# Kernel tuning notes

Measured on AMD Instinct MI355X. Metric: run time of the kernel, lower is better.

## Reference

```python
import jax, jax.numpy as jnp
import numpy as np

ALPHA = 0.65
KERNEL_RADIUS = 3
BIG = 1e30  # stand-in for +inf in morphological (tropical) convolution


def morphological_kernel(finsler_params, kernel_radius, alpha):
    """Sample the fractional morphological kernel on a (2r+1)x(2r+1) grid.

    F_c(x,y) = sqrt(x^2+y^2) * exp(-sum_k params[c,k] * B_k(theta)) with
    B_1=cos(t), B_2=sin(t), B_3=cos(2t), ... (circular harmonics).
    Kernel for the alpha-homogeneous HJB PDE (t=1):
      k(x) = nu_a * F(x)^(2a/(2a-1)),  nu_a = (2a-1)*(2a)^(-2a/(2a-1)).
    """
    r = kernel_radius
    coords = jnp.arange(-r, r + 1, dtype=finsler_params.dtype)
    yy = coords[:, None]  # [kh,1]
    xx = coords[None, :]  # [1,kw]
    rho = jnp.sqrt(xx * xx + yy * yy)              # [kh,kw]
    theta = jnp.arctan2(yy + 0 * xx, xx + 0 * yy)  # [kh,kw]
    K = finsler_params.shape[1]
    ks = np.arange(1, K + 1)
    freqs = jnp.asarray((ks + 1) // 2, dtype=finsler_params.dtype)  # 1,1,2,2,...
    ang = freqs[:, None, None] * theta[None]                        # [K,kh,kw]
    is_cos = jnp.asarray(ks % 2 == 1)[:, None, None]
    basis = jnp.where(is_cos, jnp.cos(ang), jnp.sin(ang))           # [K,kh,kw]
    F = rho[None] * jnp.exp(-jnp.einsum('ck,kij->cij', finsler_params, basis))  # [C,kh,kw]
    p = 2.0 * alpha / (2.0 * alpha - 1.0)
    nu = (2.0 * alpha - 1.0) * (2.0 * alpha) ** (-p)
    return nu * F ** p  # zero at origin since p>0


def morphological_convolution(u, kernel):
    """out[b,c,y,x] = min_{dy,dx} u[b,c,y+dy,x+dx] + kernel[c,dy+r,dx+r].
    Scan over the (2r+1)^2 stencil offsets with a running min (no huge patches)."""
    B, C, H, W = u.shape
    kh, kw = kernel.shape[1], kernel.shape[2]
    r = kh // 2
    pad = jnp.pad(u, ((0, 0), (0, 0), (r, r), (r, r)), constant_values=BIG)
    kflat = kernel.reshape(C, kh * kw)
    dys, dxs = jnp.meshgrid(jnp.arange(kh), jnp.arange(kw), indexing='ij')
    offs = jnp.stack([dys.reshape(-1), dxs.reshape(-1)], axis=-1)  # [kh*kw,2]

    def step(carry, i):
        dy, dx = offs[i, 0], offs[i, 1]
        sl = jax.lax.dynamic_slice(pad, (0, 0, dy, dx), (B, C, H, W))
        cand = sl + kflat[:, i][None, :, None, None]
        return jnp.minimum(carry, cand), None

    init = jnp.full((B, C, H, W), BIG, u.dtype)
    out, _ = jax.lax.scan(step, init, jnp.arange(kh * kw))
    return out


def convection(u, c):
    """Translation-equivariant transport: out(x) = u(x - c_channel), bilinear
    interpolation, replicate boundary. c[:,0]=x-shift, c[:,1]=y-shift."""
    B, C, H, W = u.shape
    gy = jnp.arange(H, dtype=u.dtype)[None, :, None] - c[:, 1][:, None, None]  # [C,H,1]
    gx = jnp.arange(W, dtype=u.dtype)[None, None, :] - c[:, 0][:, None, None]  # [C,1,W]
    y0 = jnp.floor(gy)
    x0 = jnp.floor(gx)
    wy = gy - y0  # [C,H,1]
    wx = gx - x0  # [C,1,W]
    y0i = jnp.clip(y0.astype(jnp.int32), 0, H - 1)
    y1i = jnp.clip(y0i + 1, 0, H - 1)
    x0i = jnp.clip(x0.astype(jnp.int32), 0, W - 1)
    x1i = jnp.clip(x0i + 1, 0, W - 1)
    ci = jnp.arange(C)[:, None, None]

    def gather(yi, xi):  # yi:[C,H,1], xi:[C,1,W] -> [B,C,H,W]
        return u[:, ci, yi, xi]

    return ((1 - wy) * (1 - wx) * gather(y0i, x0i)
            + (1 - wy) * wx * gather(y0i, x1i)
            + wy * (1 - wx) * gather(y1i, x0i)
            + wy * wx * gather(y1i, x1i))


def cde_pde_layer(x, c, finsler_dil, finsler_ero, weight):
    u = convection(x, c)
    k_dil = morphological_kernel(finsler_dil, KERNEL_RADIUS, ALPHA)
    u = -morphological_convolution(-u, k_dil)           # fractional dilation
    k_ero = morphological_kernel(finsler_ero, KERNEL_RADIUS, ALPHA)
    u = morphological_convolution(u, k_ero)             # fractional erosion
    return jnp.einsum('bihw,io->bohw', u, weight)       # linear channel mix


def setup_inputs() -> dict:
    key = jax.random.key(0)
    k1, k2, k3, k4, k5 = jax.random.split(key, 5)
    B, Cin, Cout, H, W, K = 16, 32, 32, 256, 256, 4
    x = jax.random.normal(k1, (B, Cin, H, W), dtype=jnp.float32)
    c = jax.random.normal(k2, (Cin, 2), dtype=jnp.float32)  # ~kaiming-uniform scale
    finsler_dil = jax.random.uniform(k3, (Cin, K), minval=-1.0, maxval=1.0, dtype=jnp.float32)
    finsler_ero = jax.random.uniform(k4, (Cin, K), minval=-1.0, maxval=1.0, dtype=jnp.float32)
    weight = jax.random.normal(k5, (Cin, Cout), dtype=jnp.float32) / np.sqrt(Cin)
    return {"x": x, "c": c, "finsler_dil": finsler_dil, "finsler_ero": finsler_ero, "weight": weight}


def reference(x, c, finsler_dil, finsler_ero, weight):
    return cde_pde_layer(x, c, finsler_dil, finsler_ero, weight)
```

## Files before the change

kernel.cpp:

```cpp
#include <hip/hip_runtime.h>
#include <math.h>

#define HH 256
#define WW 256
#define NB 16
#define NC 32
#define RAD 3
#define KWID 7
#define NTAPS 49
#define TILE 64
#define CW 76
#define CH 76
#define BUFH (CH * CW + 16)
#define BIGF 1e30f
#define PADF  -57344.0f
#define TAPCLAMP 57344.0f
#define HBB 0x7B80u

typedef _Float16 h2 __attribute__((ext_vector_type(2)));

static __device__ __forceinline__ h2 h2_u(unsigned int u) {
    union { unsigned int u; h2 h; } cv; cv.u = u; return cv.h;
}
static __device__ __forceinline__ unsigned int u_h2(h2 h) {
    union { unsigned int u; h2 h; } cv; cv.h = h; return cv.u;
}

__global__ void kgen_kernel(const float* __restrict__ fd,
                            const float* __restrict__ fe,
                            unsigned int* __restrict__ kd,
                            unsigned int* __restrict__ ke) {
    const int c = blockIdx.x;
    const int t = threadIdx.x;
    if (t >= NTAPS) return;
    const int dy = t / KWID - RAD;
    const int dx = t % KWID - RAD;
    const double rho = sqrt((double)(dx * dx + dy * dy));
    const double th  = atan2((double)dy, (double)dx);
    const double alpha = 0.65;
    const double p  = 2.0 * alpha / (2.0 * alpha - 1.0);
    const double nu = (2.0 * alpha - 1.0) * pow(2.0 * alpha, -p);
    const double b1 = cos(th), b2 = sin(th), b3 = cos(2.0 * th), b4 = sin(2.0 * th);
    double s, F;
    s = (double)fd[c * 4 + 0] * b1 + (double)fd[c * 4 + 1] * b2
      + (double)fd[c * 4 + 2] * b3 + (double)fd[c * 4 + 3] * b4;
    F = rho * exp(-s);
    {
        const float kv = fminf((float)(nu * pow(F, p)), TAPCLAMP);
        union { _Float16 h; unsigned short u; } cv; cv.h = (_Float16)(-kv);
        kd[c * NTAPS + t] = (unsigned int)cv.u | ((unsigned int)cv.u << 16);
    }
    s = (double)fe[c * 4 + 0] * b1 + (double)fe[c * 4 + 1] * b2
      + (double)fe[c * 4 + 2] * b3 + (double)fe[c * 4 + 3] * b4;
    F = rho * exp(-s);
    {
        const float kv = fminf((float)(nu * pow(F, p)), TAPCLAMP);
        union { _Float16 h; unsigned short u; } cv; cv.h = (_Float16)(kv);
        ke[c * NTAPS + t] = (unsigned int)cv.u | ((unsigned int)cv.u << 16);
    }
}

__global__ __launch_bounds__(256, 8) void cde_stencil_kernel(
    const float* __restrict__ xin, const float* __restrict__ csh,
    const unsigned int* __restrict__ kdil, const unsigned int* __restrict__ kero,
    float* __restrict__ uout)
{
    __shared__ __align__(16) _Float16 bufh[BUFH];

    const int tid = threadIdx.x;
    const int tileId = blockIdx.x;
    const int c = blockIdx.y;
    const int b = blockIdx.z;
    const int ty0 = (tileId >> 2) * TILE;
    const int tx0 = (tileId & 3) * TILE;

    const float cx = csh[c * 2 + 0];
    const float cy = csh[c * 2 + 1];
    const float* __restrict__ xb = xin + (((size_t)b * NC + c) << 16);

    const float mcx = -cx, mcy = -cy;
    const float fx0 = floorf(mcx), fy0 = floorf(mcy);
    const float wxf = mcx - fx0, wyf = mcy - fy0;
    const int IX = (int)fx0, IY = (int)fy0;
    const float w00 = (1.f - wyf) * (1.f - wxf);
    const float w01 = (1.f - wyf) * wxf;
    const float w10 = wyf * (1.f - wxf);
    const float w11 = wyf * wxf;

    {
        int row = tid / CW;
        int col = tid - row * CW;
        for (int idx = tid; idx < CH * CW; idx += 256) {
            const int gy = ty0 - 6 + row;
            const int gx = tx0 - 6 + col;
            float v = PADF;
            if (gy >= 0 && gy < HH && gx >= 0 && gx < WW) {
                const int y0 = min(max(gy + IY, 0), HH - 1);
                const int y1 = min(y0 + 1, HH - 1);
                const int x0 = min(max(gx + IX, 0), WW - 1);
                const int x1 = min(x0 + 1, WW - 1);
                const float a00 = xb[(y0 << 8) + x0];
                const float a01 = xb[(y0 << 8) + x1];
                const float a10 = xb[(y1 << 8) + x0];
                const float a11 = xb[(y1 << 8) + x1];
                v = w00 * a00 + w01 * a01 + w10 * a10 + w11 * a11;
            }
            bufh[idx] = (_Float16)v;
            col += 28; row += 3;
            if (col >= CW) { col -= CW; ++row; }
        }
    }
    __syncthreads();

    h2 acc2[5][2];
    int dc0 = 0, dr0 = 0;
    const bool act2 = (tid < 252);
    {
        const unsigned int* __restrict__ kdc = kdil + c * NTAPS;
        unsigned int ta[NTAPS];
        #pragma unroll
        for (int t = 0; t < NTAPS; ++t) ta[t] = kdc[t];

        if (act2) {
            dc0 = (tid % 18) * 4;
            dr0 = (tid / 18) * 5;

            const _Float16 NINF = (_Float16)(-65504.0f);
            #pragma unroll
            for (int i = 0; i < 5; ++i) {
                acc2[i][0] = (h2){NINF, NINF};
                acc2[i][1] = (h2){NINF, NINF};
            }

            const int rb = dr0 * CW + dc0;
            #pragma unroll
            for (int rr = 0; rr < 11; ++rr) {
                const int base = rb + rr * CW;
                const uint2 A = *reinterpret_cast<const uint2*>(&bufh[base]);
                const uint2 B = *reinterpret_cast<const uint2*>(&bufh[base + 4]);
                const unsigned int w4 = *reinterpret_cast<const unsigned int*>(&bufh[base + 8]);
                const unsigned int w[5] = {A.x, A.y, B.x, B.y, w4};
                unsigned int sh[4];
                #pragma unroll
                for (int j = 0; j < 4; ++j)
                    sh[j] = __builtin_amdgcn_alignbit(w[j + 1], w[j], 16);
                const unsigned int seq0[7] = {w[0], sh[0], w[1], sh[1], w[2], sh[2], w[3]};
                const unsigned int seq1[7] = {w[1], sh[1], w[2], sh[2], w[3], sh[3], w[4]};
                #pragma unroll
                for (int i = 0; i < 5; ++i) {
                    const int ky = rr - i;
                    if (ky < 0 || ky > 6) continue;
                    const int kb = ky * KWID;
                    h2 a0 = acc2[i][0], a1 = acc2[i][1];
                    #pragma unroll
                    for (int kx = 0; kx < 7; ++kx) {
                        const h2 k2 = h2_u(ta[kb + kx]);
                        a0 = __builtin_elementwise_max(a0, h2_u(seq0[kx]) + k2);
                        a1 = __builtin_elementwise_max(a1, h2_u(seq1[kx]) + k2);
                    }
                    acc2[i][0] = a0; acc2[i][1] = a1;
                }
            }
        }
    }
    __syncthreads();

    if (act2) {
        const int gxb = tx0 - 3 + dc0;
        #pragma unroll
        for (int i = 0; i < 5; ++i) {
            const int dr = dr0 + i;
            const int gy = ty0 - 3 + dr;
            const bool rOK = (gy >= 0) && (gy < HH);
            unsigned int m0 = u_h2(acc2[i][0]);
            unsigned int m1 = u_h2(acc2[i][1]);
            if (!(rOK && gxb + 0 >= 0 && gxb + 0 < WW)) m0 = (m0 & 0xFFFF0000u) | HBB;
            if (!(rOK && gxb + 1 >= 0 && gxb + 1 < WW)) m0 = (m0 & 0x0000FFFFu) | (HBB << 16);
            if (!(rOK && gxb + 2 >= 0 && gxb + 2 < WW)) m1 = (m1 & 0xFFFF0000u) | HBB;
            if (!(rOK && gxb + 3 >= 0 && gxb + 3 < WW)) m1 = (m1 & 0x0000FFFFu) | (HBB << 16);
            uint2 st; st.x = m0; st.y = m1;
            *reinterpret_cast<uint2*>(&bufh[dr * CW + dc0]) = st;
        }
    }
    __syncthreads();

    {
        const unsigned int* __restrict__ kec = kero + c * NTAPS;
        unsigned int te[NTAPS];
        #pragma unroll
        for (int t = 0; t < NTAPS; ++t) te[t] = kec[t];

        const int ec0 = (tid & 15) * 4;
        const int er0 = (tid >> 4) * 4;

        h2 acc[4][2];
        const _Float16 PINF = (_Float16)(65504.0f);
        #pragma unroll
        for (int i = 0; i < 4; ++i) {
            acc[i][0] = (h2){PINF, PINF};
            acc[i][1] = (h2){PINF, PINF};
        }

        const int rb = er0 * CW + ec0;
        #pragma unroll
        for (int rr = 0; rr < 10; ++rr) {
            const int base = rb + rr * CW;
            const uint2 A = *reinterpret_cast<const uint2*>(&bufh[base]);
            const uint2 B = *reinterpret_cast<const uint2*>(&bufh[base + 4]);
            const unsigned int w4 = *reinterpret_cast<const unsigned int*>(&bufh[base + 8]);
            const unsigned int w[5] = {A.x, A.y, B.x, B.y, w4};
            unsigned int sh[4];
            #pragma unroll
            for (int j = 0; j < 4; ++j)
                sh[j] = __builtin_amdgcn_alignbit(w[j + 1], w[j], 16);
            const unsigned int seq0[7] = {w[0], sh[0], w[1], sh[1], w[2], sh[2], w[3]};
            const unsigned int seq1[7] = {w[1], sh[1], w[2], sh[2], w[3], sh[3], w[4]};
            #pragma unroll
            for (int i = 0; i < 4; ++i) {
                const int ky = rr - i;
                if (ky < 0 || ky > 6) continue;
                const int kb = ky * KWID;
                h2 a0 = acc[i][0], a1 = acc[i][1];
                #pragma unroll
                for (int kx = 0; kx < 7; ++kx) {
                    const h2 k2 = h2_u(te[kb + kx]);
                    a0 = __builtin_elementwise_min(a0, h2_u(seq0[kx]) + k2);
                    a1 = __builtin_elementwise_min(a1, h2_u(seq1[kx]) + k2);
                }
                acc[i][0] = a0; acc[i][1] = a1;
            }
        }

        float* __restrict__ ob = uout + (((size_t)b * NC + c) << 16);
        #pragma unroll
        for (int i = 0; i < 4; ++i) {
            float4 st;
            st.x = (float)acc[i][0].x; st.y = (float)acc[i][0].y;
            st.z = (float)acc[i][1].x; st.w = (float)acc[i][1].y;
            *reinterpret_cast<float4*>(&ob[((ty0 + er0 + i) << 8) + tx0 + ec0]) = st;
        }
    }
}

#define PXS 128
__global__ __launch_bounds__(256) void mix_kernel(float* __restrict__ u,
                                                  const float* __restrict__ wmat) {
    __shared__ float s[NC * PXS];

    const int tid = threadIdx.x;
    const int strip = blockIdx.x;
    const int b = blockIdx.y;
    float* __restrict__ ub = u + ((size_t)b << 21) + strip * PXS;

    #pragma unroll
    for (int k = 0; k < 4; ++k) {
        const int idx = tid + k * 256;
        const int i = idx >> 5;
        const int q = idx & 31;
        const float4 v = *reinterpret_cast<const float4*>(ub + (i << 16) + (q << 2));
        *reinterpret_cast<float4*>(&s[idx << 2]) = v;
    }
    __syncthreads();

    const int lane = tid & 63;
    const int wv = __builtin_amdgcn_readfirstlane(tid) >> 6;
    const int o0 = wv * 8;

    float2 acc[8];
    #pragma unroll
    for (int o = 0; o < 8; ++o) { acc[o].x = 0.f; acc[o].y = 0.f; }

    #pragma unroll
    for (int i = 0; i < NC; ++i) {
        const float2 v = *reinterpret_cast<const float2*>(&s[i * PXS + 2 * lane]);
        const float* __restrict__ wr = wmat + i * NC + o0;
        #pragma unroll
        for (int o = 0; o < 8; ++o) {
            const float w = wr[o];
            acc[o].x = fmaf(v.x, w, acc[o].x);
            acc[o].y = fmaf(v.y, w, acc[o].y);
        }
    }

    #pragma unroll
    for (int o = 0; o < 8; ++o) {
        *reinterpret_cast<float2*>(ub + ((size_t)(o0 + o) << 16) + 2 * lane) = acc[o];
    }
}

extern "C" void kernel_launch(void* const* d_in, const int* in_sizes, int n_in,
                              void* d_out, int out_size, void* d_ws, size_t ws_size,
                              hipStream_t stream) {
    const float* x  = (const float*)d_in[0];
    const float* c  = (const float*)d_in[1];
    const float* fd = (const float*)d_in[2];
    const float* fe = (const float*)d_in[3];
    const float* w  = (const float*)d_in[4];
    float* out = (float*)d_out;

    unsigned int* kd = (unsigned int*)d_ws;
    unsigned int* ke = kd + NC * NTAPS;

    kgen_kernel<<<dim3(NC), dim3(64), 0, stream>>>(fd, fe, kd, ke);
    cde_stencil_kernel<<<dim3(16, NC, NB), dim3(256), 0, stream>>>(x, c, kd, ke, out);
    mix_kernel<<<dim3((HH * WW) / PXS, NB), dim3(256), 0, stream>>>(out, w);
}
```

Before: 426.5 us.

## Store stencil intermediate as fp16 in workspace and reuse rows in bilinear shift

The stencil kernel can now write its result as packed fp16 into a workspace buffer, and a new mix kernel reads that fp16 intermediate and writes fp32 output. This halves the intermediate's write and read traffic between the two kernels. The shift/bilinear load phase is also restructured so each thread walks a column and reuses the previously interpolated row, cutting global loads roughly in half. The fp16 path only runs if the workspace is large enough (about 64 MB); otherwise it falls back to the fp32 path.

```diff
diff --git a/kernel.cpp b/kernel.cpp
--- a/kernel.cpp
+++ b/kernel.cpp
@@ -12,7 +12,6 @@
 #define CW 76
 #define CH 76
 #define BUFH (CH * CW + 16)
-#define BIGF 1e30f
 #define PADF  -57344.0f
 #define TAPCLAMP 57344.0f
 #define HBB 0x7B80u
@@ -63,7 +62,7 @@
 __global__ __launch_bounds__(256, 8) void cde_stencil_kernel(
     const float* __restrict__ xin, const float* __restrict__ csh,
     const unsigned int* __restrict__ kdil, const unsigned int* __restrict__ kero,
-    float* __restrict__ uout)
+    float* __restrict__ uout32, unsigned short* __restrict__ uout16, const int mode)
 {
     __shared__ __align__(16) _Float16 bufh[BUFH];
 
@@ -82,32 +81,41 @@
     const float fx0 = floorf(mcx), fy0 = floorf(mcy);
     const float wxf = mcx - fx0, wyf = mcy - fy0;
     const int IX = (int)fx0, IY = (int)fy0;
-    const float w00 = (1.f - wyf) * (1.f - wxf);
-    const float w01 = (1.f - wyf) * wxf;
-    const float w10 = wyf * (1.f - wxf);
-    const float w11 = wyf * wxf;
-
-    {
-        int row = tid / CW;
-        int col = tid - row * CW;
-        for (int idx = tid; idx < CH * CW; idx += 256) {
-            const int gy = ty0 - 6 + row;
-            const int gx = tx0 - 6 + col;
+
+    if (tid < 228) {
+        const int col = tid % 76;
+        const int g   = tid / 76;
+        const int r0 = (g == 0) ? 0 : (g == 1 ? 26 : 51);
+        const int r1 = (g == 0) ? 26 : (g == 1 ? 51 : 76);
+        const int gx = tx0 - 6 + col;
+        const bool xok = (gx >= 0) && (gx < WW);
+        const int x0 = min(max(gx + IX, 0), WW - 1);
+        const int x1 = min(x0 + 1, WW - 1);
+
+        float rowA = 0.f, rowB = 0.f;
+        int prevY1 = -12345;
+        for (int r = r0; r < r1; ++r) {
+            const int gy = ty0 - 6 + r;
             float v = PADF;
-            if (gy >= 0 && gy < HH && gx >= 0 && gx < WW) {
+            if (xok && gy >= 0 && gy < HH) {
                 const int y0 = min(max(gy + IY, 0), HH - 1);
                 const int y1 = min(y0 + 1, HH - 1);
-                const int x0 = min(max(gx + IX, 0), WW - 1);
-                const int x1 = min(x0 + 1, WW - 1);
-                const float a00 = xb[(y0 << 8) + x0];
-                const float a01 = xb[(y0 << 8) + x1];
-                const float a10 = xb[(y1 << 8) + x0];
-                const float a11 = xb[(y1 << 8) + x1];
-                v = w00 * a00 + w01 * a01 + w10 * a10 + w11 * a11;
-            }
-            bufh[idx] = (_Float16)v;
-            col += 28; row += 3;
-            if (col >= CW) { col -= CW; ++row; }
+                if (y0 == prevY1) {
+                    rowA = rowB;
+                } else {
+                    const float a = xb[(y0 << 8) + x0];
+                    const float bb = xb[(y0 << 8) + x1];
+                    rowA = a + wxf * (bb - a);
+                }
+                {
+                    const float a = xb[(y1 << 8) + x0];
+                    const float bb = xb[(y1 << 8) + x1];
+                    rowB = a + wxf * (bb - a);
+                }
+                prevY1 = y1;
+                v = rowA + wyf * (rowB - rowA);
+            }
+            bufh[r * CW + col] = (_Float16)v;
         }
     }
     __syncthreads();
@@ -231,18 +239,77 @@
             }
         }
 
-        float* __restrict__ ob = uout + (((size_t)b * NC + c) << 16);
-        #pragma unroll
-        for (int i = 0; i < 4; ++i) {
-            float4 st;
-            st.x = (float)acc[i][0].x; st.y = (float)acc[i][0].y;
-            st.z = (float)acc[i][1].x; st.w = (float)acc[i][1].y;
-            *reinterpret_cast<float4*>(&ob[((ty0 + er0 + i) << 8) + tx0 + ec0]) = st;
+        if (mode) {
+            unsigned short* __restrict__ ob = uout16 + (((size_t)b * NC + c) << 16);
+            #pragma unroll
+            for (int i = 0; i < 4; ++i) {
+                uint2 st; st.x = u_h2(acc[i][0]); st.y = u_h2(acc[i][1]);
+                *reinterpret_cast<uint2*>(&ob[((ty0 + er0 + i) << 8) + tx0 + ec0]) = st;
+            }
+        } else {
+            float* __restrict__ ob = uout32 + (((size_t)b * NC + c) << 16);
+            #pragma unroll
+            for (int i = 0; i < 4; ++i) {
+                float4 st;
+                st.x = (float)acc[i][0].x; st.y = (float)acc[i][0].y;
+                st.z = (float)acc[i][1].x; st.w = (float)acc[i][1].y;
+                *reinterpret_cast<float4*>(&ob[((ty0 + er0 + i) << 8) + tx0 + ec0]) = st;
+            }
         }
     }
 }
 
 #define PXS 128
+__global__ __launch_bounds__(256) void mixh_kernel(const unsigned short* __restrict__ uh,
+                                                   float* __restrict__ out,
+                                                   const float* __restrict__ wmat) {
+    __shared__ unsigned short s[NC * PXS];
+
+    const int tid = threadIdx.x;
+    const int strip = blockIdx.x;
+    const int b = blockIdx.y;
+    const unsigned short* __restrict__ ubh = uh + ((size_t)b << 21) + strip * PXS;
+
+    #pragma unroll
+    for (int k = 0; k < 2; ++k) {
+        const int idx = tid + k * 256;
+        const int i = idx >> 4;
+        const int q = idx & 15;
+        const uint4 v = *reinterpret_cast<const uint4*>(ubh + ((size_t)i << 16) + (q << 3));
+        *reinterpret_cast<uint4*>(&s[(i << 7) + (q << 3)]) = v;
+    }
+    __syncthreads();
+
+    const int lane = tid & 63;
+    const int wv = __builtin_amdgcn_readfirstlane(tid) >> 6;
+    const int o0 = wv * 8;
+
+    float2 acc[8];
+    #pragma unroll
+    for (int o = 0; o < 8; ++o) { acc[o].x = 0.f; acc[o].y = 0.f; }
+
+    #pragma unroll
+    for (int i = 0; i < NC; ++i) {
+        const unsigned int hv = *reinterpret_cast<const unsigned int*>(&s[(i << 7) + 2 * lane]);
+        const h2 hh = h2_u(hv);
+        const float vx = (float)hh.x;
+        const float vy = (float)hh.y;
+        const float* __restrict__ wr = wmat + i * NC + o0;
+        #pragma unroll
+        for (int o = 0; o < 8; ++o) {
+            const float w = wr[o];
+            acc[o].x = fmaf(vx, w, acc[o].x);
+            acc[o].y = fmaf(vy, w, acc[o].y);
+        }
+    }
+
+    float* __restrict__ ob = out + ((size_t)b << 21) + strip * PXS;
+    #pragma unroll
+    for (int o = 0; o < 8; ++o) {
+        *reinterpret_cast<float2*>(ob + ((size_t)(o0 + o) << 16) + 2 * lane) = acc[o];
+    }
+}
+
 __global__ __launch_bounds__(256) void mix_kernel(float* __restrict__ u,
                                                   const float* __restrict__ wmat) {
     __shared__ float s[NC * PXS];
@@ -301,7 +368,16 @@
     unsigned int* kd = (unsigned int*)d_ws;
     unsigned int* ke = kd + NC * NTAPS;
 
+    const size_t uhOff   = 16384;
+    const size_t uhBytes = (size_t)NB * NC * HH * WW * 2;
+    const bool f16path = (ws_size >= uhOff + uhBytes);
+    unsigned short* uh = (unsigned short*)((char*)d_ws + uhOff);
+
     kgen_kernel<<<dim3(NC), dim3(64), 0, stream>>>(fd, fe, kd, ke);
-    cde_stencil_kernel<<<dim3(16, NC, NB), dim3(256), 0, stream>>>(x, c, kd, ke, out);
-    mix_kernel<<<dim3((HH * WW) / PXS, NB), dim3(256), 0, stream>>>(out, w);
-}
+    cde_stencil_kernel<<<dim3(16, NC, NB), dim3(256), 0, stream>>>(
+        x, c, kd, ke, out, uh, f16path ? 1 : 0);
+    if (f16path)
+        mixh_kernel<<<dim3((HH * WW) / PXS, NB), dim3(256), 0, stream>>>(uh, out, w);
+    else
+        mix_kernel<<<dim3((HH * WW) / PXS, NB), dim3(256), 0, stream>>>(out, w);
+}
```

Result: faster. 391.4 us (-8.2%).
